# Kernel tuning notes

Measured on AMD Instinct MI355X. Metric: run time of the kernel, lower is better.

The kernel has to match this reference:

```python
import jax, jax.numpy as jnp
import numpy as np

HIDDEN = 768
HEADS = 12
HEAD_DIM = HIDDEN // HEADS
SCALE = HEAD_DIM ** -0.5
GAMMA = 0.5  # non-trainable nn.Parameter in the original module


def setup_inputs() -> dict:
    key = jax.random.key(0)
    k1, k2, k3, k4 = jax.random.split(key, 4)
    B, N, C = 2, 2048, HIDDEN
    x = jax.random.normal(k1, (B, N, C), dtype=jnp.float32)
    w_qkv = jax.random.normal(k2, (3 * C, C), dtype=jnp.float32) * 0.02
    w_out = jax.random.normal(k3, (C, C), dtype=jnp.float32) * 0.02
    b_out = jax.random.normal(k4, (C,), dtype=jnp.float32) * 0.02
    return {"x": x, "w_qkv": w_qkv, "w_out": w_out, "b_out": b_out}


def _spa_mask(N: int, dtype) -> jnp.ndarray:
    # has_cls=False path: mask[k, j] = GAMMA iff j % (N//4) == k % (N//4), else 1.
    NUM = N // 4
    rows = jnp.arange(N) % NUM  # [N]
    cols = jnp.arange(N) % NUM  # [N]
    return jnp.where(rows[:, None] == cols[None, :],
                     jnp.asarray(GAMMA, dtype), jnp.asarray(1.0, dtype))  # [N, N]


def reference(x, w_qkv, w_out, b_out):
    B, N, C = x.shape
    H, D = HEADS, HEAD_DIM
    # qkv projection (no bias): [B,N,3C] -> [3,B,H,N,D] per 'b n (qkv h d) -> qkv b h n d'
    qkv = jnp.einsum('bnc,fc->bnf', x, w_qkv).reshape(B, N, 3, H, D)
    qkv = jnp.transpose(qkv, (2, 0, 3, 1, 4))
    q, k, v = qkv[0], qkv[1], qkv[2]
    # first softmax over scaled scores
    att = jax.nn.softmax(jnp.einsum('bhxd,bhyd->bhxy', q, k) * SCALE, axis=-1)
    # structured block-periodic mask multiply, then second softmax
    mask = _spa_mask(N, att.dtype)  # [N,N], broadcasts over [B,H,N,N]
    att = jax.nn.softmax(att * mask, axis=-1)
    # value weighting and output projection
    out = jnp.einsum('bhxy,bhyd->bhxd', att, v)  # [B,H,N,D]
    out = jnp.transpose(out, (0, 2, 1, 3)).reshape(B, N, C)  # b h n d -> b n (h d)
    return jnp.einsum('bnc,oc->bno', out, w_out) + b_out
```

## Files before the change

kernel.cpp:

```cpp
#include <hip/hip_runtime.h>
#include <hip/hip_bf16.h>
#include <cstdint>
#include <cstddef>

typedef __attribute__((ext_vector_type(8))) short short8;
typedef __attribute__((ext_vector_type(4))) short short4v;
typedef __attribute__((ext_vector_type(4))) float f32x4;
typedef __attribute__((ext_vector_type(16))) float f32x16;

#define HH 12
#define DD 64
#define NN 2048
#define CC 768
#define QSCALE 0.18033688011112042f

__device__ __forceinline__ float bf2f(short s) {
  union { uint32_t u; float f; } v;
  v.u = ((uint32_t)(uint16_t)s) << 16;
  return v.f;
}
__device__ __forceinline__ short f2bf(float f) {
  union { float f; uint32_t u; } v; v.f = f;
  uint32_t r = v.u + 0x7FFFu + ((v.u >> 16) & 1u);
  return (short)(r >> 16);
}
__device__ __forceinline__ uint32_t cvtpk(float a, float b) {
  uint32_t r;
  asm("v_cvt_pk_bf16_f32 %0, %1, %2" : "=v"(r) : "v"(a), "v"(b));
  return r;
}

__global__ __launch_bounds__(256)
void norm_k(const float* __restrict__ s0, const float* __restrict__ s1,
            const float* __restrict__ s2,
            short* __restrict__ d0, short* __restrict__ d1,
            short* __restrict__ d2)
{
  const int bid = blockIdx.x;
  const float* src; short* dst; int base;
  if (bid < 1536)      { src = s0; dst = d0; base = bid; }
  else if (bid < 2400) { src = s1; dst = d1; base = bid - 1536; }
  else                 { src = s2; dst = d2; base = bid - 2400; }
  const int idx = (base * 256 + (int)threadIdx.x) * 8;
  const float* sf = src + idx;
  f32x4 a = *(const f32x4*)sf;
  f32x4 b = *(const f32x4*)(sf + 4);
  short8 o;
  o[0] = f2bf(a[0]); o[1] = f2bf(a[1]); o[2] = f2bf(a[2]); o[3] = f2bf(a[3]);
  o[4] = f2bf(b[0]); o[5] = f2bf(b[1]); o[6] = f2bf(b[2]); o[7] = f2bf(b[3]);
  *(short8*)(dst + idx) = o;
}

template <int MODE>
__global__ __launch_bounds__(256, 2)
void gemm_k(const short* __restrict__ A, const short* __restrict__ W,
            const float* __restrict__ bias,
            short* __restrict__ O0, short* __restrict__ O1, short* __restrict__ O2,
            float* __restrict__ Of)
{
  __shared__ __align__(16) short lA[128 * 64];
  __shared__ __align__(16) short lB[128 * 64];
  const int tid = threadIdx.x;
  const int w = tid >> 6, l = tid & 63;
  const int lq = l & 15, lh = l >> 4;
  const int m0 = blockIdx.y * 128;
  const int f0 = blockIdx.x * 128;
  const int seg = tid & 7;
  const int rbase = tid >> 3;

  f32x4 acc[4][4] = {};

  for (int kb = 0; kb < CC; kb += 64) {
    __syncthreads();
#pragma unroll
    for (int j = 0; j < 4; ++j) {
      const int row = j * 32 + rbase;
      const int dst = row * 128 + ((seg * 16) ^ ((row & 7) << 4));
      *(short8*)((char*)lA + dst) =
          *(const short8*)(A + (size_t)(m0 + row) * CC + kb + seg * 8);
      *(short8*)((char*)lB + dst) =
          *(const short8*)(W + (size_t)(f0 + row) * CC + kb + seg * 8);
    }
    __syncthreads();
    const int wr = (w >> 1) * 64, wc = (w & 1) * 64;
#pragma unroll
    for (int c = 0; c < 2; ++c) {
      short8 af[4], bfr[4];
#pragma unroll
      for (int i = 0; i < 4; ++i) {
        const int rowA = wr + i * 16 + lq;
        af[i] = *(const short8*)((char*)lA + rowA * 128 +
                                 ((c * 64 + lh * 16) ^ ((rowA & 7) << 4)));
        const int rowB = wc + i * 16 + lq;
        bfr[i] = *(const short8*)((char*)lB + rowB * 128 +
                                  ((c * 64 + lh * 16) ^ ((rowB & 7) << 4)));
      }
#pragma unroll
      for (int mi = 0; mi < 4; ++mi)
#pragma unroll
        for (int ni = 0; ni < 4; ++ni)
          acc[mi][ni] = __builtin_amdgcn_mfma_f32_16x16x32_bf16(
              af[mi], bfr[ni], acc[mi][ni], 0, 0, 0);
    }
  }

  const int wr = (w >> 1) * 64, wc = (w & 1) * 64;
#pragma unroll
  for (int ni = 0; ni < 4; ++ni) {
    const int fb = f0 + wc + ni * 16;
    if (MODE == 0) {
      const int which = fb / CC;
      const int hd = fb - which * CC;
      const int h = hd >> 6;
      const int d = (hd & 63) + lq;
#pragma unroll
      for (int mi = 0; mi < 4; ++mi) {
        const int mb = m0 + wr + mi * 16 + 4 * lh;
        const int b = mb >> 11;
        const int n = mb & 2047;
        if (which == 0) {
#pragma unroll
          for (int r = 0; r < 4; ++r)
            O0[(((size_t)(b * HH + h) * NN) + n + r) * DD + d] =
                f2bf(acc[mi][ni][r] * QSCALE);
        } else if (which == 1) {
#pragma unroll
          for (int r = 0; r < 4; ++r)
            O1[(((size_t)(b * HH + h) * NN) + n + r) * DD + d] =
                f2bf(acc[mi][ni][r]);
        } else {
          short4v pk;
#pragma unroll
          for (int r = 0; r < 4; ++r) pk[r] = f2bf(acc[mi][ni][r]);
          *(short4v*)(O2 + ((size_t)(b * HH + h) * DD + d) * NN + n) = pk;
        }
      }
    } else {
      const float bv = bias[fb + lq];
#pragma unroll
      for (int mi = 0; mi < 4; ++mi) {
        const int mb = m0 + wr + mi * 16 + 4 * lh;
#pragma unroll
        for (int r = 0; r < 4; ++r)
          Of[(size_t)(mb + r) * CC + fb + lq] = acc[mi][ni][r] + bv;
      }
    }
  }
}

__global__ __launch_bounds__(256)
void colsum_k(const short* __restrict__ VT, float* __restrict__ cs)
{
  const int bh = blockIdx.x, t = threadIdx.x;
  const int d = t >> 2, part = t & 3;
  const short* p = VT + ((size_t)bh * DD + d) * NN + part * 512;
  float s = 0.f;
  for (int i = 0; i < 512; i += 8) {
    short8 v = *(const short8*)(p + i);
#pragma unroll
    for (int e = 0; e < 8; ++e) s += bf2f(v[e]);
  }
  s += __shfl_xor(s, 1);
  s += __shfl_xor(s, 2);
  if (part == 0) cs[bh * DD + d] = s;
}

__global__ __launch_bounds__(256, 3)
void attn_k(const short* __restrict__ Qb, const short* __restrict__ Kb,
            const short* __restrict__ VT, const float* __restrict__ cs,
            short* __restrict__ AO)
{
  __shared__ __align__(16) char smem[32768];
  float* comb  = (float*)smem;
  float* combL = comb + 4096;
  float* combM = comb + 4160;

  const int tid = threadIdx.x;
  const int w = tid >> 6, l = tid & 63;
  const int lq = l & 31, hi = l >> 5;
  const int qp = w & 1;
  const int kc = w >> 1;

  const int bid = (int)blockIdx.x;
  const int sbid = (bid & 7) * 96 + (bid >> 3);
  const int bh = sbid >> 5;
  const int qblk = sbid & 31;

  const short* Qh = Qb + (size_t)bh * NN * DD;
  const short* Kh = Kb + (size_t)bh * NN * DD;
  const short* Vh = VT + (size_t)bh * DD * NN;

  const int qw = qblk * 64 + qp * 32;
  const int qg = qw + lq;

  short8 qf[4];
#pragma unroll
  for (int c = 0; c < 4; ++c)
    qf[c] = *(const short8*)(Qh + (size_t)qg * DD + c * 16 + hi * 8);

  f32x16 pv[2] = {};
  float l1x[4] = {};
  float mc = 0.f;

  const int lt = tid & 127;
  const int seg = lt & 7, rbase = lt >> 3;
  const int cbase = kc * 16384;
  int sdstK[4], sdstV[4], ksrc[4], vsrc[4];
#pragma unroll
  for (int j = 0; j < 4; ++j) {
    const int row = j * 16 + rbase;
    const int sw = row * 128 + ((seg * 16) ^ ((row & 7) << 4));
    sdstK[j] = cbase + sw;
    sdstV[j] = cbase + 8192 + sw;
    ksrc[j] = row * DD + seg * 8;
    vsrc[j] = row * NN + seg * 8;
  }
  int kaddr[8], vaddr[8];
#pragma unroll
  for (int kg = 0; kg < 2; ++kg) {
    const int rowK = kg * 32 + lq;
#pragma unroll
    for (int c = 0; c < 4; ++c)
      kaddr[kg * 4 + c] =
          cbase + rowK * 128 + ((c * 32 + hi * 16) ^ ((rowK & 7) << 4));
  }
#pragma unroll
  for (int dg = 0; dg < 2; ++dg) {
    const int rowV = dg * 32 + lq;
#pragma unroll
    for (int ch = 0; ch < 4; ++ch)
      vaddr[ch * 2 + dg] =
          cbase + 8192 + rowV * 128 + ((ch * 32 + hi * 16) ^ ((rowV & 7) << 4));
  }

  const int kb0 = kc * (NN / 2);
  for (int t = 0; t < NN / 2; t += 64) {
    const int kb = kb0 + t;
    __syncthreads();
#pragma unroll
    for (int j = 0; j < 4; ++j) {
      *(short8*)(smem + sdstK[j]) = *(const short8*)(Kh + (size_t)kb * DD + ksrc[j]);
      *(short8*)(smem + sdstV[j]) = *(const short8*)(Vh + kb + vsrc[j]);
    }
    __syncthreads();

    f32x16 sacc[2] = {};
#pragma unroll
    for (int kg = 0; kg < 2; ++kg)
#pragma unroll
      for (int c = 0; c < 4; ++c) {
        short8 kf = *(const short8*)(smem + kaddr[kg * 4 + c]);
        sacc[kg] = __builtin_amdgcn_mfma_f32_32x32x16_bf16(kf, qf[c], sacc[kg], 0, 0, 0);
      }

    uint32_t dwv[2][8];
    const int u = (qw - kb) & 511;
    if (u < 64 || u > 480) {
      const int delta = (qg - kb) & 511;
      int mreg = -1;
      if (delta < 64 && (((delta >> 2) & 1) == hi))
        mreg = (delta >> 5) * 16 + (delta & 3) + (((delta & 31) >> 3) << 2);
#pragma unroll
      for (int kg = 0; kg < 2; ++kg) {
        float uv[16];
#pragma unroll
        for (int r = 0; r < 16; ++r) {
          float e = __builtin_exp2f(sacc[kg][r]);
          l1x[r & 3] += e;
          const bool m = (kg * 16 + r) == mreg;
          mc += m ? e : 0.f;
          uv[r] = m ? 0.5f * e : e;
        }
#pragma unroll
        for (int j2 = 0; j2 < 8; ++j2)
          dwv[kg][j2] = cvtpk(uv[2 * j2], uv[2 * j2 + 1]);
      }
    } else {
#pragma unroll
      for (int kg = 0; kg < 2; ++kg) {
        float uv[16];
#pragma unroll
        for (int r = 0; r < 16; ++r) {
          const float e = __builtin_exp2f(sacc[kg][r]);
          l1x[r & 3] += e;
          uv[r] = e;
        }
#pragma unroll
        for (int j2 = 0; j2 < 8; ++j2)
          dwv[kg][j2] = cvtpk(uv[2 * j2], uv[2 * j2 + 1]);
      }
    }

    short8 pa[4];
#pragma unroll
    for (int kg = 0; kg < 2; ++kg)
#pragma unroll
      for (int half = 0; half < 2; ++half) {
        uint32_t a0 = dwv[kg][4 * half + 0], a1 = dwv[kg][4 * half + 1];
        uint32_t a2 = dwv[kg][4 * half + 2], a3 = dwv[kg][4 * half + 3];
        asm("v_permlane32_swap_b32 %0, %1" : "+v"(a0), "+v"(a2));
        asm("v_permlane32_swap_b32 %0, %1" : "+v"(a1), "+v"(a3));
        union { uint32_t u4[4]; short8 s; } pk;
        pk.u4[0] = a0; pk.u4[1] = a1; pk.u4[2] = a2; pk.u4[3] = a3;
        pa[kg * 2 + half] = pk.s;
      }

#pragma unroll
    for (int ch = 0; ch < 4; ++ch)
#pragma unroll
      for (int dg = 0; dg < 2; ++dg) {
        short8 vf = *(const short8*)(smem + vaddr[ch * 2 + dg]);
        pv[dg] = __builtin_amdgcn_mfma_f32_32x32x16_bf16(pa[ch], vf, pv[dg], 0, 0, 0);
      }
  }

  float l1 = (l1x[0] + l1x[1]) + (l1x[2] + l1x[3]);
  l1 += __shfl_xor(l1, 32);
  mc += __shfl_xor(mc, 32);

  __syncthreads();
  if (kc == 1) {
#pragma unroll
    for (int dg = 0; dg < 2; ++dg)
#pragma unroll
      for (int r = 0; r < 16; ++r) {
        const int qrow = (r & 3) + 8 * (r >> 2) + 4 * hi;
        comb[(qp * 32 + qrow) * 64 + dg * 32 + lq] = pv[dg][r];
      }
    if (hi == 0) {
      combL[qp * 32 + lq] = l1;
      combM[qp * 32 + lq] = mc;
    }
  }
  __syncthreads();
  if (kc == 0) {
    const float l1t = l1 + combL[qp * 32 + lq];
    const float mct = mc + combM[qp * 32 + lq];
    const float s1t = l1t - 0.5f * mct;
    const int b = bh / HH, h = bh - b * HH;
#pragma unroll
    for (int r = 0; r < 16; ++r) {
      const int qrow = (r & 3) + 8 * (r >> 2) + 4 * hi;
      const float l1r = __shfl(l1t, qrow);
      const float s1r = __shfl(s1t, qrow);
      const float rden = 1.f / (2048.f * l1r + s1r);
      const int n = qw + qrow;
#pragma unroll
      for (int dg = 0; dg < 2; ++dg) {
        const int d = dg * 32 + lq;
        const float pvt = pv[dg][r] + comb[(qp * 32 + qrow) * 64 + d];
        const float csv = cs[bh * DD + d];
        AO[((size_t)(b * NN + n)) * CC + h * DD + d] =
            f2bf((csv * l1r + pvt) * rden);
      }
    }
  }
}

extern "C" void kernel_launch(void* const* d_in, const int* in_sizes, int n_in,
                              void* d_out, int out_size, void* d_ws, size_t ws_size,
                              hipStream_t stream)
{
  (void)in_sizes; (void)n_in; (void)out_size;
  float* out = (float*)d_out;

  const size_t HD = (size_t)2 * HH * NN * DD;
  const size_t NX = 3145728, NW = 1769472, NO = 589824;
  const size_t need = (4 * HD + NX + NW + NO) * sizeof(short)
                    + (size_t)2 * HH * DD * sizeof(float) + 64;
  if (ws_size < need) return;

  short* Qb = (short*)d_ws;
  short* Kb = Qb + HD;
  short* VT = Kb + HD;
  short* AO = VT + HD;
  float* cs = (float*)(AO + HD);
  short* xb  = (short*)(cs + 2 * HH * DD);
  short* wqb = xb + NX;
  short* wob = wqb + NW;

  dim3 blk(256);
  norm_k<<<dim3(2688), blk, 0, stream>>>((const float*)d_in[0],
                                         (const float*)d_in[1],
                                         (const float*)d_in[2],
                                         xb, wqb, wob);
  gemm_k<0><<<dim3(2304 / 128, 4096 / 128), blk, 0, stream>>>(
      xb, wqb, nullptr, Qb, Kb, VT, nullptr);
  colsum_k<<<dim3(2 * HH), blk, 0, stream>>>(VT, cs);
  attn_k<<<dim3(24 * 32), blk, 0, stream>>>(Qb, Kb, VT, cs, AO);
  gemm_k<1><<<dim3(CC / 128, 4096 / 128), blk, 0, stream>>>(
      AO, wob, (const float*)d_in[3], nullptr, nullptr, nullptr, out);
}
```

Baseline: 110.2 us.

## Prefetch next K/V tile into registers and use direct global-to-LDS loads in GEMM

In the attention kernel, the next K/V tile is now loaded into registers while the current tile is being computed, and written to LDS after a barrier at the end of each iteration. This hides global load latency behind the MFMA work. The GEMM staging switches to global_load_lds (when the builtin exists), with the swizzle applied on the source side, so data skips the register round trip. s_setprio is raised around the MFMA blocks. The cost is extra registers for the prefetch buffers, which may lower occupancy, plus the risk that the swizzle mapping differs from the original layout.

```diff
diff --git a/kernel.cpp b/kernel.cpp
--- a/kernel.cpp
+++ b/kernel.cpp
@@ -13,6 +13,19 @@
 #define NN 2048
 #define CC 768
 #define QSCALE 0.18033688011112042f
+
+#if defined(__has_builtin)
+#if __has_builtin(__builtin_amdgcn_global_load_lds)
+#define HAVE_GLOAD_LDS 1
+#endif
+#endif
+
+#ifdef HAVE_GLOAD_LDS
+#define GL16(gp, lp)                                                         \
+  __builtin_amdgcn_global_load_lds(                                         \
+      (__attribute__((address_space(1))) void*)(size_t)(const void*)(gp),   \
+      (__attribute__((address_space(3))) void*)(lp), 16, 0, 0)
+#endif
 
 __device__ __forceinline__ float bf2f(short s) {
   union { uint32_t u; float f; } v;
@@ -65,13 +78,28 @@
   const int lq = l & 15, lh = l >> 4;
   const int m0 = blockIdx.y * 128;
   const int f0 = blockIdx.x * 128;
+
+#ifdef HAVE_GLOAD_LDS
+  const int lrow = l >> 3;
+  const int gseg = ((l & 7) ^ lrow) * 8;
+#else
   const int seg = tid & 7;
   const int rbase = tid >> 3;
+#endif
 
   f32x4 acc[4][4] = {};
 
   for (int kb = 0; kb < CC; kb += 64) {
     __syncthreads();
+#ifdef HAVE_GLOAD_LDS
+#pragma unroll
+    for (int j = 0; j < 4; ++j) {
+      const int rw = j * 32 + w * 8;
+      const int row = rw + lrow;
+      GL16(A + (size_t)(m0 + row) * CC + kb + gseg, &lA[rw * 64]);
+      GL16(W + (size_t)(f0 + row) * CC + kb + gseg, &lB[rw * 64]);
+    }
+#else
 #pragma unroll
     for (int j = 0; j < 4; ++j) {
       const int row = j * 32 + rbase;
@@ -81,6 +109,7 @@
       *(short8*)((char*)lB + dst) =
           *(const short8*)(W + (size_t)(f0 + row) * CC + kb + seg * 8);
     }
+#endif
     __syncthreads();
     const int wr = (w >> 1) * 64, wc = (w & 1) * 64;
 #pragma unroll
@@ -234,17 +263,32 @@
   }
 
   const int kb0 = kc * (NN / 2);
+
+  short8 kreg[4], vreg[4];
+#pragma unroll
+  for (int j = 0; j < 4; ++j) {
+    kreg[j] = *(const short8*)(Kh + (size_t)kb0 * DD + ksrc[j]);
+    vreg[j] = *(const short8*)(Vh + kb0 + vsrc[j]);
+  }
+#pragma unroll
+  for (int j = 0; j < 4; ++j) {
+    *(short8*)(smem + sdstK[j]) = kreg[j];
+    *(short8*)(smem + sdstV[j]) = vreg[j];
+  }
+
   for (int t = 0; t < NN / 2; t += 64) {
     const int kb = kb0 + t;
     __syncthreads();
-#pragma unroll
-    for (int j = 0; j < 4; ++j) {
-      *(short8*)(smem + sdstK[j]) = *(const short8*)(Kh + (size_t)kb * DD + ksrc[j]);
-      *(short8*)(smem + sdstV[j]) = *(const short8*)(Vh + kb + vsrc[j]);
-    }
-    __syncthreads();
+    if (t + 64 < NN / 2) {
+#pragma unroll
+      for (int j = 0; j < 4; ++j) {
+        kreg[j] = *(const short8*)(Kh + (size_t)(kb + 64) * DD + ksrc[j]);
+        vreg[j] = *(const short8*)(Vh + kb + 64 + vsrc[j]);
+      }
+    }
 
     f32x16 sacc[2] = {};
+    __builtin_amdgcn_s_setprio(1);
 #pragma unroll
     for (int kg = 0; kg < 2; ++kg)
 #pragma unroll
@@ -252,6 +296,7 @@
         short8 kf = *(const short8*)(smem + kaddr[kg * 4 + c]);
         sacc[kg] = __builtin_amdgcn_mfma_f32_32x32x16_bf16(kf, qf[c], sacc[kg], 0, 0, 0);
       }
+    __builtin_amdgcn_s_setprio(0);
 
     uint32_t dwv[2][8];
     const int u = (qw - kb) & 511;
@@ -305,6 +350,7 @@
         pa[kg * 2 + half] = pk.s;
       }
 
+    __builtin_amdgcn_s_setprio(1);
 #pragma unroll
     for (int ch = 0; ch < 4; ++ch)
 #pragma unroll
@@ -312,6 +358,16 @@
         short8 vf = *(const short8*)(smem + vaddr[ch * 2 + dg]);
         pv[dg] = __builtin_amdgcn_mfma_f32_32x32x16_bf16(pa[ch], vf, pv[dg], 0, 0, 0);
       }
+    __builtin_amdgcn_s_setprio(0);
+
+    __syncthreads();
+    if (t + 64 < NN / 2) {
+#pragma unroll
+      for (int j = 0; j < 4; ++j) {
+        *(short8*)(smem + sdstK[j]) = kreg[j];
+        *(short8*)(smem + sdstV[j]) = vreg[j];
+      }
+    }
   }
 
   float l1 = (l1x[0] + l1x[1]) + (l1x[2] + l1x[3]);
```

Result: slower. 152.1 us (+38.1%).
